# Kernel tuning notes

Measured on AMD Instinct MI355X. Metric: run time of the kernel, lower is better.

Reference implementation:

```python
import jax, jax.numpy as jnp
import numpy as np

N_LOW = 50000
N_HIGH = 200000
E = 1000000       # number of (i, j, k) triplets from the radius search
K = 27            # 3x3x3 voxel kernel cells
C_IN = 128
C_OUT = 128


def setup_inputs() -> dict:
    key = jax.random.key(0)
    k0, k1, k2, k3, k4, k5 = jax.random.split(key, 6)
    x_low = jax.random.normal(k0, (N_LOW, C_IN), dtype=jnp.float32)
    # PointConv3d weight: one [C_OUT, C_IN] matrix per kernel cell, kaiming-ish scale
    weight = jax.random.normal(k1, (K, C_OUT, C_IN), dtype=jnp.float32) * (1.0 / np.sqrt(C_IN))
    bias = jax.random.normal(k2, (C_OUT,), dtype=jnp.float32) * 0.01
    i_high = jax.random.randint(k3, (E,), 0, N_HIGH, dtype=jnp.int32)
    j_low = jax.random.randint(k4, (E,), 0, N_LOW, dtype=jnp.int32)
    k_cell = jax.random.randint(k5, (E,), 0, K, dtype=jnp.int32)
    return {"x_low": x_low, "weight": weight, "bias": bias,
            "i_high": i_high, "j_low": j_low, "k": k_cell, "n_high": N_HIGH}


def reference(x_low, weight, bias, i_high, j_low, k, n_high):
    # Sparse point convolution: out[i] += weight[k] @ x_low[j], then + bias.
    # Efficient form: transform every low-res point by all K kernel matrices once
    # (dense GEMM), then gather the (j, k) entry per triplet and scatter-add by i.
    y = jnp.einsum('nc,koc->nko', x_low, weight)       # [N_low, K, C_out]
    msg = y[j_low, k]                                  # [E, C_out] gather
    out = jnp.zeros((n_high, weight.shape[1]), dtype=x_low.dtype)
    out = out.at[i_high].add(msg)                      # scatter-add to high-res points
    return out + bias
```

## Files before the change

kernel.cpp:

```cpp
#include <hip/hip_runtime.h>

typedef _Float16 half8 __attribute__((ext_vector_type(8)));
typedef _Float16 half4v __attribute__((ext_vector_type(4)));
typedef _Float16 half2v __attribute__((ext_vector_type(2)));
typedef float f32x4 __attribute__((ext_vector_type(4)));

#define CAP 32
#define OVF_MAX 4096


__global__ void cvt_inputs(const float* __restrict__ x, const float* __restrict__ w,
                           const float* __restrict__ bias,
                           _Float16* __restrict__ Xh, _Float16* __restrict__ Wh,
                           float* __restrict__ biasPerm,
                           int xv4, int xt4, int w4) {
    int i = blockIdx.x * blockDim.x + threadIdx.x;
    if (i < xt4) {
        float4 v = (i < xv4) ? reinterpret_cast<const float4*>(x)[i]
                             : make_float4(0.f, 0.f, 0.f, 0.f);
        half4v h; h[0]=(_Float16)v.x; h[1]=(_Float16)v.y; h[2]=(_Float16)v.z; h[3]=(_Float16)v.w;
        reinterpret_cast<half4v*>(Xh)[i] = h;
    } else if (i < xt4 + w4) {
        int j = i - xt4;
        float4 v = reinterpret_cast<const float4*>(w)[j];
        half4v h; h[0]=(_Float16)v.x; h[1]=(_Float16)v.y; h[2]=(_Float16)v.z; h[3]=(_Float16)v.w;
        reinterpret_cast<half4v*>(Wh)[j] = h;
    } else if (i < xt4 + w4 + 32) {
        int j2 = i - xt4 - w4;
        int wn = j2 >> 4, mrow = j2 & 15;
        float4 v;
        v.x = bias[wn * 64 + 0 * 16 + mrow];
        v.y = bias[wn * 64 + 1 * 16 + mrow];
        v.z = bias[wn * 64 + 2 * 16 + mrow];
        v.w = bias[wn * 64 + 3 * 16 + mrow];
        reinterpret_cast<float4*>(biasPerm)[j2] = v;
    }
}

__global__ void zero_ints(int* __restrict__ p, int n) {
    int i = blockIdx.x * blockDim.x + threadIdx.x;
    if (i < n) p[i] = 0;
}

__global__ void init_bias(float* __restrict__ out, const float* __restrict__ bias, int n4) {
    int i = blockIdx.x * blockDim.x + threadIdx.x;
    if (i >= n4) return;
    reinterpret_cast<float4*>(out)[i] = reinterpret_cast<const float4*>(bias)[i & 31];
}

__global__ __launch_bounds__(256) void mask_store(
    const int* __restrict__ jl, const int* __restrict__ kc,
    unsigned char* __restrict__ maskB, int Mpad, int E) {
    int e = blockIdx.x * blockDim.x + threadIdx.x;
    if (e >= E) return;
    maskB[(size_t)kc[e] * Mpad + jl[e]] = 1;
}

__global__ __launch_bounds__(256) void gemm_xw(
    const _Float16* __restrict__ Xh,
    const _Float16* __restrict__ Wh,
    _Float16* __restrict__ Y,
    const unsigned char* __restrict__ maskB,
    int Mpad, int ldY,
    const int* __restrict__ ih, const int* __restrict__ jl,
    const int* __restrict__ kc,
    int* __restrict__ counts, int* __restrict__ bucket,
    int* __restrict__ ovf_cnt, int* __restrict__ ovf_list, int E) {
    __shared__ ushort sA[128 * 128];
    __shared__ ushort sB[128 * 128];
    const int tid = threadIdx.x;
    const int m0 = blockIdx.x * 128;
    const int kc0 = blockIdx.y * 3;
    const ushort* Ag = (const ushort*)Xh + (size_t)m0 * 128;

#pragma unroll
    for (int it = 0; it < 8; ++it) {
        int p = it * 256 + tid;
        int row = p >> 4, cpos = p & 15;
        int csrc = cpos ^ (row & 15);
        __builtin_amdgcn_global_load_lds(
            (const __attribute__((address_space(1))) void*)(Ag + row * 128 + csrc * 8),
            (__attribute__((address_space(3))) void*)(&sA[row * 128 + cpos * 8]), 16, 0, 0);
    }
    {
        const ushort* Bg = (const ushort*)Wh + (size_t)kc0 * 128 * 128;
#pragma unroll
        for (int it = 0; it < 8; ++it) {
            int p = it * 256 + tid;
            int row = p >> 4, cpos = p & 15;
            int csrc = cpos ^ (row & 15);
            __builtin_amdgcn_global_load_lds(
                (const __attribute__((address_space(1))) void*)(Bg + row * 128 + csrc * 8),
                (__attribute__((address_space(3))) void*)(&sB[row * 128 + cpos * 8]), 16, 0, 0);
        }
    }

    {
        int nb = gridDim.x * gridDim.y;
        int bid = blockIdx.y * gridDim.x + blockIdx.x;
        int per = (E + nb - 1) / nb;
        int e0 = bid * per;
        int e1 = e0 + per; if (e1 > E) e1 = E;
        for (int e = e0 + tid; e < e1; e += 256) {
            int i = ih[e];
            int off = jl[e] * ldY + kc[e] * 128;
            int pos = atomicAdd(&counts[i], 1);
            if (pos < CAP) {
                bucket[(size_t)i * CAP + pos] = off;
            } else {
                int o = atomicAdd(ovf_cnt, 1);
                if (o < OVF_MAX) { ovf_list[2 * o] = i; ovf_list[2 * o + 1] = off; }
            }
        }
    }

    __builtin_amdgcn_s_waitcnt(0);
    __syncthreads();

    const int lane = tid & 63;
    const int wid = tid >> 6;
    const int wm = wid & 1, wn = wid >> 1;
    const int mrow = lane & 15;
    const int g = lane >> 4;

    for (int kk = 0; kk < 3; ++kk) {
        f32x4 acc[4][4] = {};
#pragma unroll
        for (int kb = 0; kb < 4; ++kb) {
            half8 af[4], bf[4];
#pragma unroll
            for (int t = 0; t < 4; ++t) {
                int cpos8 = ((kb * 4 + g) ^ mrow) * 8;
                int ra = wm * 64 + t * 16 + mrow;
                af[t] = *reinterpret_cast<const half8*>(&sA[ra * 128 + cpos8]);
                int rb = wn * 64 + t * 16 + mrow;
                bf[t] = *reinterpret_cast<const half8*>(&sB[rb * 128 + cpos8]);
            }
#pragma unroll
            for (int mt = 0; mt < 4; ++mt)
#pragma unroll
                for (int nt = 0; nt < 4; ++nt)
                    acc[mt][nt] = __builtin_amdgcn_mfma_f32_16x16x32_f16(
                        af[mt], bf[nt], acc[mt][nt], 0, 0, 0);
        }
        __syncthreads();
        if (kk < 2) {
            const ushort* Bg = (const ushort*)Wh + (size_t)(kc0 + kk + 1) * 128 * 128;
#pragma unroll
            for (int it = 0; it < 8; ++it) {
                int p = it * 256 + tid;
                int row = p >> 4, cpos = p & 15;
                int csrc = cpos ^ (row & 15);
                __builtin_amdgcn_global_load_lds(
                    (const __attribute__((address_space(1))) void*)(Bg + row * 128 + csrc * 8),
                    (__attribute__((address_space(3))) void*)(&sB[row * 128 + cpos * 8]), 16, 0, 0);
            }
        }
        const unsigned char* mBp = maskB + (size_t)(kc0 + kk) * Mpad + m0 + wm * 64;
        _Float16* Yt = Y + (size_t)m0 * ldY + (kc0 + kk) * 128 + wn * 64 + mrow * 4;
#pragma unroll
        for (int mt = 0; mt < 4; ++mt) {
            unsigned mw = *reinterpret_cast<const unsigned*>(mBp + mt * 16 + g * 4);
            if (mw) {
#pragma unroll
                for (int r = 0; r < 4; ++r) {
                    if ((mw >> (8 * r)) & 0xFFu) {
                        int row = wm * 64 + mt * 16 + g * 4 + r;
                        half4v hv;
#pragma unroll
                        for (int nt = 0; nt < 4; ++nt) hv[nt] = (_Float16)acc[mt][nt][r];
                        *reinterpret_cast<half4v*>(Yt + (size_t)row * ldY) = hv;
                    }
                }
            }
        }
        if (kk < 2) {
            __builtin_amdgcn_s_waitcnt(0);
            __syncthreads();
        }
    }
}

__global__ __launch_bounds__(256) void gather_out(
    const _Float16* __restrict__ Y, const int* __restrict__ counts,
    const int* __restrict__ bucket, const float* __restrict__ biasPerm,
    float* __restrict__ out, int Nhigh, int zoff) {
    int wave = (blockIdx.x * blockDim.x + threadIdx.x) >> 6;
    int lane = threadIdx.x & 63;
    int p = lane >> 4;
    int sub = lane & 15;
    int i = wave * 4 + p;
    bool act = i < Nhigh;
    int iC = act ? i : 0;
    int nb = counts[iC];
    if (nb > CAP) nb = CAP;
    const int* bk = bucket + (size_t)iC * CAP;
    int offsA = bk[sub];
    int offsB = bk[sub + 16];
    float4 b0 = reinterpret_cast<const float4*>(biasPerm)[sub * 2];
    float4 b1 = reinterpret_cast<const float4*>(biasPerm)[sub * 2 + 1];
    float acc[8] = {b0.x, b0.y, b0.z, b0.w, b1.x, b1.y, b1.z, b1.w};

    int nmax = nb;
    nmax = max(nmax, __shfl_xor(nmax, 16));
    nmax = max(nmax, __shfl_xor(nmax, 32));

    for (int e0 = 0; e0 < nmax; e0 += 4) {
#pragma unroll
        for (int u = 0; u < 4; ++u) {
            int e = e0 + u;
            int off = (e < 16) ? __shfl(offsA, p * 16 + (e & 15))
                               : __shfl(offsB, p * 16 + (e & 15));
            bool valid = act && (e < nb);
            off = valid ? off : zoff;
            half8 h = *reinterpret_cast<const half8*>(Y + (size_t)off + sub * 8);
#pragma unroll
            for (int t = 0; t < 8; ++t) acc[t] += (float)h[t];
        }
    }
    if (act) {
        float* op = out + (size_t)i * 128;
        int obase = (sub >> 3) * 64 + (sub & 7) * 2;
#pragma unroll
        for (int t = 0; t < 8; ++t)
            op[obase + (t & 3) * 16 + (t >> 2)] = acc[t];
    }
}

__global__ void apply_overflow(const int* __restrict__ ovf_cnt, const int* __restrict__ ovf_list,
                               const _Float16* __restrict__ Y, float* __restrict__ out) {
    int n = *ovf_cnt;
    if (n > OVF_MAX) n = OVF_MAX;
    int lane = threadIdx.x & 63;
    int w = threadIdx.x >> 6;
    int o0p = 2 * lane, o1p = 2 * lane + 1;
    int o0 = (o0p >> 6) * 64 + (o0p & 3) * 16 + ((o0p >> 2) & 15);
    int o1 = (o1p >> 6) * 64 + (o1p & 3) * 16 + ((o1p >> 2) & 15);
    for (int o = w; o < n; o += 4) {
        int i = ovf_list[2 * o], off = ovf_list[2 * o + 1];
        half2v h = *reinterpret_cast<const half2v*>(Y + (size_t)off + lane * 2);
        float* dst = out + (size_t)i * 128;
        unsafeAtomicAdd(dst + o0, (float)h[0]);
        unsafeAtomicAdd(dst + o1, (float)h[1]);
    }
}

__global__ void fallback_edge(const float* __restrict__ x, const float* __restrict__ w,
                              const int* __restrict__ ih, const int* __restrict__ jl,
                              const int* __restrict__ kc, float* __restrict__ out, int E) {
    int e = blockIdx.x;
    if (e >= E) return;
    int lane = threadIdx.x;
    int i = ih[e], j = jl[e], k = kc[e];
    const float* xr = x + (size_t)j * 128;
    const float* wk = w + (size_t)k * 128 * 128;
    float s0 = 0.f, s1 = 0.f;
    for (int c = 0; c < 128; ++c) {
        float xv = xr[c];
        s0 += wk[(size_t)lane * 128 + c] * xv;
        s1 += wk[(size_t)(lane + 64) * 128 + c] * xv;
    }
    unsafeAtomicAdd(&out[(size_t)i * 128 + lane], s0);
    unsafeAtomicAdd(&out[(size_t)i * 128 + 64 + lane], s1);
}

extern "C" void kernel_launch(void* const* d_in, const int* in_sizes, int n_in,
                              void* d_out, int out_size, void* d_ws, size_t ws_size,
                              hipStream_t stream) {
    const float* x    = (const float*)d_in[0];
    const float* w    = (const float*)d_in[1];
    const float* bias = (const float*)d_in[2];
    const int*   ih   = (const int*)d_in[3];
    const int*   jl   = (const int*)d_in[4];
    const int*   kc   = (const int*)d_in[5];
    float* out = (float*)d_out;

    const int C = 128;
    const int Nlow = in_sizes[0] / C;
    const int K = in_sizes[1] / (C * C);
    const int E = in_sizes[3];
    const int ldY = K * C;
    const int Nhigh = out_size / C;

    const int mtiles = (Nlow + 127) / 128;
    const int Mpad = mtiles * 128;

    size_t off = 0;
    auto alloc = [&](size_t bytes) { size_t o = off; off = (off + bytes + 255) & ~(size_t)255; return o; };
    size_t xh_off   = alloc((size_t)Mpad * C * 2);
    size_t wh_off   = alloc((size_t)K * C * C * 2);
    size_t bp_off   = alloc((size_t)C * 4);
    size_t cnt_off  = alloc(((size_t)Nhigh + 1) * 4 + (size_t)Mpad * K);
    size_t ovl_off  = alloc((size_t)OVF_MAX * 2 * 4);
    size_t bkt_off  = alloc((size_t)Nhigh * CAP * 4);
    size_t y_off    = alloc(((size_t)Mpad * ldY + C) * 2);
    size_t need_sort = off;

    _Float16* Xh = (_Float16*)((char*)d_ws + xh_off);
    _Float16* Wh = (_Float16*)((char*)d_ws + wh_off);
    float* biasPerm = (float*)((char*)d_ws + bp_off);
    int* counts  = (int*)((char*)d_ws + cnt_off);
    int* ovf_cnt = counts + Nhigh;
    unsigned char* maskB = (unsigned char*)(counts + Nhigh + 1);
    int* ovf_lst = (int*)((char*)d_ws + ovl_off);
    int* bucket  = (int*)((char*)d_ws + bkt_off);
    _Float16* Y  = (_Float16*)((char*)d_ws + y_off);
    const int zoff = Mpad * ldY;

    if (ws_size >= need_sort && (K % 3) == 0) {
        int xv4 = Nlow * C / 4, xt4 = Mpad * C / 4;
        int w4 = K * C * C / 4;
        cvt_inputs<<<(xt4 + w4 + 32 + 255) / 256, 256, 0, stream>>>(
            x, w, bias, Xh, Wh, biasPerm, xv4, xt4, w4);
        int nz = Nhigh + 1 + (Mpad * K) / 4;
        zero_ints<<<(nz + 255) / 256, 256, 0, stream>>>(counts, nz);
        zero_ints<<<1, 64, 0, stream>>>((int*)(Y + (size_t)zoff), C / 2);
        mask_store<<<(E + 255) / 256, 256, 0, stream>>>(jl, kc, maskB, Mpad, E);
        gemm_xw<<<dim3(mtiles, K / 3), 256, 0, stream>>>(
            Xh, Wh, Y, maskB, Mpad, ldY,
            ih, jl, kc, counts, bucket, ovf_cnt, ovf_lst, E);
        gather_out<<<(Nhigh + 15) / 16, 256, 0, stream>>>(
            Y, counts, bucket, biasPerm, out, Nhigh, zoff);
        apply_overflow<<<1, 256, 0, stream>>>(ovf_cnt, ovf_lst, Y, out);
    } else {
        int n4out = out_size / 4;
        init_bias<<<(n4out + 255) / 256, 256, 0, stream>>>(out, bias, n4out);
        fallback_edge<<<E, 64, 0, stream>>>(x, w, ih, jl, kc, out, E);
    }
}
```

Before: 354.6 us.

## Fuse conversion, mask and bucket build; split bucketing between prep and GEMM kernels

Merges input conversion, Y zero-pad, mask store and part of the triplet bucketing into one prep kernel, which removes two launches. The GEMM kernel now buckets exactly one triplet per thread. It issues those index loads and the atomic before its LDS wait and defers the bucket store until after the first MFMA pass, so the atomic latency is meant to overlap compute. It also drops the trailing barrier on the last iteration and doubles the gather loop unroll to 8. This adds hand-written waitcnt and scheduling barriers, and it depends on the vmcnt(4) count being correct.

```diff
diff --git a/kernel.cpp b/kernel.cpp
--- a/kernel.cpp
+++ b/kernel.cpp
@@ -9,11 +9,28 @@
 #define OVF_MAX 4096
 
 
-__global__ void cvt_inputs(const float* __restrict__ x, const float* __restrict__ w,
-                           const float* __restrict__ bias,
-                           _Float16* __restrict__ Xh, _Float16* __restrict__ Wh,
-                           float* __restrict__ biasPerm,
-                           int xv4, int xt4, int w4) {
+__global__ void zero_ints(int* __restrict__ p, int n) {
+    int i = blockIdx.x * blockDim.x + threadIdx.x;
+    if (i < n) p[i] = 0;
+}
+
+__global__ void init_bias(float* __restrict__ out, const float* __restrict__ bias, int n4) {
+    int i = blockIdx.x * blockDim.x + threadIdx.x;
+    if (i >= n4) return;
+    reinterpret_cast<float4*>(out)[i] = reinterpret_cast<const float4*>(bias)[i & 31];
+}
+
+__global__ __launch_bounds__(256) void cvt_mask(
+    const float* __restrict__ x, const float* __restrict__ w,
+    const float* __restrict__ bias,
+    _Float16* __restrict__ Xh, _Float16* __restrict__ Wh,
+    float* __restrict__ biasPerm, _Float16* __restrict__ Yz,
+    const int* __restrict__ ih, const int* __restrict__ jl,
+    const int* __restrict__ kc,
+    unsigned char* __restrict__ maskB,
+    int* __restrict__ counts, int* __restrict__ bucket,
+    int* __restrict__ ovf_cnt, int* __restrict__ ovf_list,
+    int Mpad, int ldY, int xv4, int xt4, int w4, int E, int eg) {
     int i = blockIdx.x * blockDim.x + threadIdx.x;
     if (i < xt4) {
         float4 v = (i < xv4) ? reinterpret_cast<const float4*>(x)[i]
@@ -34,26 +51,27 @@
         v.z = bias[wn * 64 + 2 * 16 + mrow];
         v.w = bias[wn * 64 + 3 * 16 + mrow];
         reinterpret_cast<float4*>(biasPerm)[j2] = v;
-    }
-}
-
-__global__ void zero_ints(int* __restrict__ p, int n) {
-    int i = blockIdx.x * blockDim.x + threadIdx.x;
-    if (i < n) p[i] = 0;
-}
-
-__global__ void init_bias(float* __restrict__ out, const float* __restrict__ bias, int n4) {
-    int i = blockIdx.x * blockDim.x + threadIdx.x;
-    if (i >= n4) return;
-    reinterpret_cast<float4*>(out)[i] = reinterpret_cast<const float4*>(bias)[i & 31];
-}
-
-__global__ __launch_bounds__(256) void mask_store(
-    const int* __restrict__ jl, const int* __restrict__ kc,
-    unsigned char* __restrict__ maskB, int Mpad, int E) {
-    int e = blockIdx.x * blockDim.x + threadIdx.x;
-    if (e >= E) return;
-    maskB[(size_t)kc[e] * Mpad + jl[e]] = 1;
+    } else if (i < xt4 + w4 + 48) {
+        int t = i - xt4 - w4 - 32;
+        reinterpret_cast<int4*>(Yz)[t] = make_int4(0, 0, 0, 0);
+    } else {
+        int e = i - (xt4 + w4 + 48);
+        if (e < E) {
+            int j = jl[e], kk = kc[e];
+            maskB[(size_t)kk * Mpad + j] = 1;
+            if (e >= eg) {
+                int ii = ih[e];
+                int off = j * ldY + kk * 128;
+                int pos = atomicAdd(&counts[ii], 1);
+                if (pos < CAP) {
+                    bucket[(size_t)ii * CAP + pos] = off;
+                } else {
+                    int o = atomicAdd(ovf_cnt, 1);
+                    if (o < OVF_MAX) { ovf_list[2 * o] = ii; ovf_list[2 * o + 1] = off; }
+                }
+            }
+        }
+    }
 }
 
 __global__ __launch_bounds__(256) void gemm_xw(
@@ -65,7 +83,7 @@
     const int* __restrict__ ih, const int* __restrict__ jl,
     const int* __restrict__ kc,
     int* __restrict__ counts, int* __restrict__ bucket,
-    int* __restrict__ ovf_cnt, int* __restrict__ ovf_list, int E) {
+    int* __restrict__ ovf_cnt, int* __restrict__ ovf_list, int eg) {
     __shared__ ushort sA[128 * 128];
     __shared__ ushort sB[128 * 128];
     const int tid = threadIdx.x;
@@ -94,28 +112,25 @@
                 (__attribute__((address_space(3))) void*)(&sB[row * 128 + cpos * 8]), 16, 0, 0);
         }
     }
-
-    {
-        int nb = gridDim.x * gridDim.y;
-        int bid = blockIdx.y * gridDim.x + blockIdx.x;
-        int per = (E + nb - 1) / nb;
-        int e0 = bid * per;
-        int e1 = e0 + per; if (e1 > E) e1 = E;
-        for (int e = e0 + tid; e < e1; e += 256) {
-            int i = ih[e];
-            int off = jl[e] * ldY + kc[e] * 128;
-            int pos = atomicAdd(&counts[i], 1);
-            if (pos < CAP) {
-                bucket[(size_t)i * CAP + pos] = off;
-            } else {
-                int o = atomicAdd(ovf_cnt, 1);
-                if (o < OVF_MAX) { ovf_list[2 * o] = i; ovf_list[2 * o + 1] = off; }
-            }
-        }
-    }
-
-    __builtin_amdgcn_s_waitcnt(0);
-    __syncthreads();
+    __builtin_amdgcn_sched_barrier(0);
+
+    const int bid = blockIdx.y * gridDim.x + blockIdx.x;
+    const bool hasE = (bid * 256) < eg;
+    int i0 = 0, off0 = 0, pos0 = CAP;
+    if (hasE) {
+        int e = bid * 256 + tid;
+        i0 = ih[e];
+        off0 = jl[e] * ldY + kc[e] * 128;
+        pos0 = atomicAdd(&counts[i0], 1);
+        __builtin_amdgcn_sched_barrier(0);
+        asm volatile("s_waitcnt vmcnt(4)" ::: "memory");
+    } else {
+        __builtin_amdgcn_sched_barrier(0);
+        asm volatile("s_waitcnt vmcnt(0)" ::: "memory");
+    }
+    __builtin_amdgcn_sched_barrier(0);
+    __builtin_amdgcn_s_barrier();
+    __builtin_amdgcn_sched_barrier(0);
 
     const int lane = tid & 63;
     const int wid = tid >> 6;
@@ -143,8 +158,9 @@
                     acc[mt][nt] = __builtin_amdgcn_mfma_f32_16x16x32_f16(
                         af[mt], bf[nt], acc[mt][nt], 0, 0, 0);
         }
-        __syncthreads();
         if (kk < 2) {
+            __builtin_amdgcn_s_barrier();
+            __builtin_amdgcn_sched_barrier(0);
             const ushort* Bg = (const ushort*)Wh + (size_t)(kc0 + kk + 1) * 128 * 128;
 #pragma unroll
             for (int it = 0; it < 8; ++it) {
@@ -154,6 +170,14 @@
                 __builtin_amdgcn_global_load_lds(
                     (const __attribute__((address_space(1))) void*)(Bg + row * 128 + csrc * 8),
                     (__attribute__((address_space(3))) void*)(&sB[row * 128 + cpos * 8]), 16, 0, 0);
+            }
+        }
+        if (kk == 0 && hasE) {
+            if (pos0 < CAP) {
+                bucket[(size_t)i0 * CAP + pos0] = off0;
+            } else {
+                int o = atomicAdd(ovf_cnt, 1);
+                if (o < OVF_MAX) { ovf_list[2 * o] = i0; ovf_list[2 * o + 1] = off0; }
             }
         }
         const unsigned char* mBp = maskB + (size_t)(kc0 + kk) * Mpad + m0 + wm * 64;
@@ -205,9 +229,9 @@
     nmax = max(nmax, __shfl_xor(nmax, 16));
     nmax = max(nmax, __shfl_xor(nmax, 32));
 
-    for (int e0 = 0; e0 < nmax; e0 += 4) {
-#pragma unroll
-        for (int u = 0; u < 4; ++u) {
+    for (int e0 = 0; e0 < nmax; e0 += 8) {
+#pragma unroll
+        for (int u = 0; u < 8; ++u) {
             int e = e0 + u;
             int off = (e < 16) ? __shfl(offsA, p * 16 + (e & 15))
                                : __shfl(offsB, p * 16 + (e & 15));
@@ -310,15 +334,23 @@
     if (ws_size >= need_sort && (K % 3) == 0) {
         int xv4 = Nlow * C / 4, xt4 = Mpad * C / 4;
         int w4 = K * C * C / 4;
-        cvt_inputs<<<(xt4 + w4 + 32 + 255) / 256, 256, 0, stream>>>(
-            x, w, bias, Xh, Wh, biasPerm, xv4, xt4, w4);
+        int nbGemm = mtiles * (K / 3);
+        long long cap256 = (long long)nbGemm * 256;
+        int eg = (E < cap256) ? (E & ~255) : (int)cap256;
+
         int nz = Nhigh + 1 + (Mpad * K) / 4;
         zero_ints<<<(nz + 255) / 256, 256, 0, stream>>>(counts, nz);
-        zero_ints<<<1, 64, 0, stream>>>((int*)(Y + (size_t)zoff), C / 2);
-        mask_store<<<(E + 255) / 256, 256, 0, stream>>>(jl, kc, maskB, Mpad, E);
+
+        int totalCvt = xt4 + w4 + 48 + E;
+        cvt_mask<<<(totalCvt + 255) / 256, 256, 0, stream>>>(
+            x, w, bias, Xh, Wh, biasPerm, Y + (size_t)zoff,
+            ih, jl, kc, maskB, counts, bucket, ovf_cnt, ovf_lst,
+            Mpad, ldY, xv4, xt4, w4, E, eg);
+
         gemm_xw<<<dim3(mtiles, K / 3), 256, 0, stream>>>(
             Xh, Wh, Y, maskB, Mpad, ldY,
-            ih, jl, kc, counts, bucket, ovf_cnt, ovf_lst, E);
+            ih, jl, kc, counts, bucket, ovf_cnt, ovf_lst, eg);
+
         gather_out<<<(Nhigh + 15) / 16, 256, 0, stream>>>(
             Y, counts, bucket, biasPerm, out, Nhigh, zoff);
         apply_overflow<<<1, 256, 0, stream>>>(ovf_cnt, ovf_lst, Y, out);
```

Result: no change. 350.3 us (-1.2%).
